# Performance work log

Hardware: AMD Instinct MI355X
Metric: run time of the kernel (lower is better)

## Reference

```python
import jax, jax.numpy as jnp
import numpy as np

V = 50257   # vocab
P = 2048    # max positions
D = 768     # hidden
H = 12      # heads
F = 3072    # 4*D ffn
NL = 12     # layers
L = 2048    # seq len
EPS = 1e-5


def setup_inputs() -> dict:
    key = jax.random.key(0)
    ks = jax.random.split(key, 12)
    r = lambda k, shp: jax.random.normal(k, shp, jnp.float32) * 0.02
    return dict(
        input_ids=jax.random.randint(ks[0], (1, L), 0, V, dtype=jnp.int32),
        attention_mask=jnp.ones((1, L), jnp.int32),
        wte=r(ks[1], (V, D)),
        wpe=r(ks[2], (P, D)),
        lnf_w=jnp.ones((D,), jnp.float32),
        lnf_b=jnp.zeros((D,), jnp.float32),
        ln1_w=jnp.ones((NL, D), jnp.float32),
        ln1_b=jnp.zeros((NL, D), jnp.float32),
        qw=r(ks[3], (NL, D, D)),
        kw=r(ks[4], (NL, D, D)),
        vw=r(ks[5], (NL, D, D)),
        ow=r(ks[6], (NL, D, D)),
        ob=jnp.zeros((NL, D), jnp.float32),
        ln2_w=jnp.ones((NL, D), jnp.float32),
        ln2_b=jnp.zeros((NL, D), jnp.float32),
        fcw=r(ks[7], (NL, D, F)),
        fcb=jnp.zeros((NL, F), jnp.float32),
        pw=r(ks[8], (NL, F, D)),
        pb=jnp.zeros((NL, D), jnp.float32),
    )


def _ln(x, w, b):
    mu = jnp.mean(x, -1, keepdims=True)
    var = jnp.mean((x - mu) ** 2, -1, keepdims=True)
    return (x - mu) * jax.lax.rsqrt(var + EPS) * w + b


def reference(input_ids, attention_mask, wte, wpe, lnf_w, lnf_b,
              ln1_w, ln1_b, qw, kw, vw, ow, ob, ln2_w, ln2_b,
              fcw, fcb, pw, pb):
    ids = input_ids.reshape(-1, input_ids.shape[-1])          # [1, L]
    pos = jnp.cumsum(attention_mask, -1) - 1
    pos = jnp.where(attention_mask == 0, 1, pos)
    h = (wte[ids] + wpe[pos])[0]                               # [L, D]

    key_valid = attention_mask[0] > 0                          # actual_length mask
    mask = jnp.tril(jnp.ones((L, L), bool)) & key_valid[None, :]  # causal+pad
    dh = D // H

    def layer(h, p):
        l1w, l1b, Wq, Wk, Wv, Wo, bo, l2w, l2b, Wf, bf, Wp, bp = p
        x = _ln(h, l1w, l1b)
        q = (x @ Wq).reshape(L, H, dh)
        k = (x @ Wk).reshape(L, H, dh)
        v = (x @ Wv).reshape(L, H, dh)
        # GPT-Neo attention: NO 1/sqrt(dh) scaling
        scores = jnp.einsum('qhd,khd->hqk', q, k)
        scores = jnp.where(mask[None], scores, jnp.float32(-1e9))
        attn = jax.nn.softmax(scores, axis=-1)
        ctx = jnp.einsum('hqk,khd->qhd', attn, v).reshape(L, D)
        h = h + ctx @ Wo + bo
        y = _ln(h, l2w, l2b)
        h = h + jax.nn.gelu(y @ Wf + bf, approximate=True) @ Wp + bp
        return h, None

    h, _ = jax.lax.scan(layer, h, (ln1_w, ln1_b, qw, kw, vw, ow, ob,
                                   ln2_w, ln2_b, fcw, fcb, pw, pb))
    return _ln(h[None, :, :], lnf_w, lnf_b)                    # [1, L, D]
```

## Files before the change

kernel.cpp:

```cpp
#include <hip/hip_runtime.h>
#include <hip/hip_bf16.h>
#include <math.h>
#include <stdint.h>

#define L 2048
#define D 768
#define H 12
#define DH 64
#define F 3072
#define NL 12
#define QKVN 2304

typedef __attribute__((ext_vector_type(8))) short bf16x8;
typedef __attribute__((ext_vector_type(4))) float f32x4;

__device__ __forceinline__ ushort f2bf(float x) {
    union { float f; uint32_t u; } c; c.f = x;
    uint32_t r = c.u + 0x7FFFu + ((c.u >> 16) & 1u);
    return (ushort)(r >> 16);
}

__device__ __forceinline__ uint32_t cvt_pk_bf16(float lo, float hi) {
    uint32_t r;
    asm("v_cvt_pk_bf16_f32 %0, %1, %2" : "=v"(r) : "v"(lo), "v"(hi));
    return r;
}

__device__ __forceinline__ bf16x8 ldfrag(const ushort* p) {
    ushort4 lo = *(const ushort4*)(p);
    ushort4 hi = *(const ushort4*)(p + 16);
    bf16x8 f;
    f[0] = (short)lo.x; f[1] = (short)lo.y; f[2] = (short)lo.z; f[3] = (short)lo.w;
    f[4] = (short)hi.x; f[5] = (short)hi.y; f[6] = (short)hi.z; f[7] = (short)hi.w;
    return f;
}

__device__ __forceinline__ float gelu_tanh(float x) {
    float c = 0.7978845608028654f;
    float inner = c * (x + 0.044715f * x * x * x);
    return 0.5f * x * (1.0f + tanhf(inner));
}

__global__ void pos_kernel(const int* __restrict__ mask, int* __restrict__ pos) {
    __shared__ int sm[L];
    for (int i = threadIdx.x; i < L; i += blockDim.x) sm[i] = mask[i];
    __syncthreads();
    int t = blockIdx.x * blockDim.x + threadIdx.x;
    if (t < L) {
        int s = 0;
        for (int j = 0; j <= t; ++j) s += sm[j];
        int p = s - 1;
        if (sm[t] == 0) p = 1;
        pos[t] = p;
    }
}

__global__ void maskb_kernel(const int* __restrict__ mask, float* __restrict__ mb) {
    int i = blockIdx.x * blockDim.x + threadIdx.x;
    if (i < L) mb[i] = mask[i] ? 0.f : -1e9f;
}

__global__ __launch_bounds__(256) void embed_kernel(const int* __restrict__ ids,
                                                    const int* __restrict__ pos,
                                                    const float* __restrict__ wte,
                                                    const float* __restrict__ wpe,
                                                    float* __restrict__ h) {
    int t = blockIdx.x;
    int id = ids[t];
    int p = pos[t];
    const float* we = wte + (size_t)id * D;
    const float* wp = wpe + (size_t)p * D;
    float* hr = h + (size_t)t * D;
#pragma unroll
    for (int i = 0; i < 3; ++i) {
        int d = threadIdx.x + i * 256;
        hr[d] = we[d] + wp[d];
    }
}

template <bool OUTBF>
__global__ __launch_bounds__(256) void ln_kernel(const float* __restrict__ in,
                                                 const float* __restrict__ w,
                                                 const float* __restrict__ b,
                                                 float* __restrict__ outF,
                                                 ushort* __restrict__ outB) {
    __shared__ float red[2][4];
    int row = blockIdx.x;
    const float* x = in + (size_t)row * D;
    int t = threadIdx.x;
    float v0 = x[t], v1 = x[t + 256], v2 = x[t + 512];
    float s = v0 + v1 + v2;
    float ss = v0 * v0 + v1 * v1 + v2 * v2;
#pragma unroll
    for (int o = 32; o; o >>= 1) {
        s += __shfl_xor(s, o);
        ss += __shfl_xor(ss, o);
    }
    int wave = t >> 6;
    if ((t & 63) == 0) { red[0][wave] = s; red[1][wave] = ss; }
    __syncthreads();
    s = red[0][0] + red[0][1] + red[0][2] + red[0][3];
    ss = red[1][0] + red[1][1] + red[1][2] + red[1][3];
    float mean = s * (1.f / D);
    float var = ss * (1.f / D) - mean * mean;
    float rstd = rsqrtf(var + 1e-5f);
#pragma unroll
    for (int i = 0; i < 3; ++i) {
        int d = t + i * 256;
        float vv = (i == 0) ? v0 : (i == 1) ? v1 : v2;
        float y = (vv - mean) * rstd * w[d] + b[d];
        if (OUTBF) outB[(size_t)row * D + d] = f2bf(y);
        else       outF[(size_t)row * D + d] = y;
    }
}

template <int S, bool OUTBF>
__global__ __launch_bounds__(256) void redln_kernel(const float* __restrict__ part,
                                                    const float* __restrict__ bias,
                                                    float* __restrict__ h,
                                                    const float* __restrict__ lnw,
                                                    const float* __restrict__ lnb,
                                                    ushort* __restrict__ outB,
                                                    float* __restrict__ outF) {
    __shared__ float red[2][4];
    int row = blockIdx.x;
    int t = threadIdx.x;
    float v[3];
    float s = 0.f, ss = 0.f;
#pragma unroll
    for (int i = 0; i < 3; ++i) {
        int d = t + i * 256;
        float x = h[(size_t)row * D + d] + bias[d];
#pragma unroll
        for (int sp = 0; sp < S; ++sp)
            x += part[((size_t)sp * L + row) * D + d];
        v[i] = x;
        h[(size_t)row * D + d] = x;
        s += x;
        ss += x * x;
    }
#pragma unroll
    for (int o = 32; o; o >>= 1) {
        s += __shfl_xor(s, o);
        ss += __shfl_xor(ss, o);
    }
    int wave = t >> 6;
    if ((t & 63) == 0) { red[0][wave] = s; red[1][wave] = ss; }
    __syncthreads();
    s = red[0][0] + red[0][1] + red[0][2] + red[0][3];
    ss = red[1][0] + red[1][1] + red[1][2] + red[1][3];
    float mean = s * (1.f / D);
    float var = ss * (1.f / D) - mean * mean;
    float rstd = rsqrtf(var + 1e-5f);
#pragma unroll
    for (int i = 0; i < 3; ++i) {
        int d = t + i * 256;
        float y = (v[i] - mean) * rstd * lnw[d] + lnb[d];
        if (OUTBF) outB[(size_t)row * D + d] = f2bf(y);
        else       outF[(size_t)row * D + d] = y;
    }
}

__global__ __launch_bounds__(256) void tcast_f32(const float* __restrict__ in,
                                                 ushort* __restrict__ out,
                                                 int K, int N,
                                                 size_t inStride, size_t outStride) {
    in += blockIdx.z * inStride;
    out += blockIdx.z * outStride;
    __shared__ float tile[64][65];
    int k0 = blockIdx.y * 64, n0 = blockIdx.x * 64;
    int t = threadIdx.x;
    int cl = t & 63, rg = t >> 6;
#pragma unroll
    for (int i = 0; i < 16; ++i) {
        int r = rg + 4 * i;
        tile[r][cl] = in[(size_t)(k0 + r) * N + n0 + cl];
    }
    __syncthreads();
#pragma unroll
    for (int i = 0; i < 16; ++i) {
        int r = rg + 4 * i;
        out[(size_t)(n0 + r) * K + k0 + cl] = f2bf(tile[cl][r]);
    }
}

template <int ACT, bool OUTBF, int SPLITK, bool VSPLIT>
__global__ __launch_bounds__(256) void gemm_bf16(const ushort* __restrict__ A,
                                                 const ushort* __restrict__ Bt,
                                                 const float* __restrict__ bias,
                                                 const float* __restrict__ resid,
                                                 float* __restrict__ outF,
                                                 ushort* __restrict__ outB,
                                                 float* __restrict__ pout,
                                                 ushort* __restrict__ vTout,
                                                 int M, int N, int K) {
    __shared__ __align__(16) char lds[32768];
    const int tid = threadIdx.x;
    const int lane = tid & 63, w = tid >> 6;
    const int wr = w >> 1, wc = w & 1;
    const int bm = blockIdx.y * 128, bn = blockIdx.x * 128;
    const int l15 = lane & 15, l4 = lane >> 4;
    const int srow = tid >> 2, c = tid & 3;
    const int blo = (c & 1) * 32 + (c >> 1) * 8;
    const int kLen = K / SPLITK;
    const int kStart = (SPLITK > 1) ? blockIdx.z * kLen : 0;

    const int sxor = (srow & 3) << 4;
    const int wo0 = srow * 64 + (blo ^ sxor);
    const int wo1 = srow * 64 + ((blo + 16) ^ sxor);
    const int rxor = (l4 * 16) ^ ((l15 & 3) << 4);
    const int aBase = (wr * 64 + l15) * 64 + rxor;
    const int bBase = (wc * 64 + l15) * 64 + rxor;

    f32x4 acc[4][4];
#pragma unroll
    for (int m = 0; m < 4; ++m)
#pragma unroll
        for (int n = 0; n < 4; ++n)
            acc[m][n] = (f32x4){0.f, 0.f, 0.f, 0.f};

    const ushort* Ag = A + (size_t)(bm + srow) * K + kStart + c * 8;
    const ushort* Ag2 = Ag + (size_t)64 * K;
    const ushort* Bg = Bt + (size_t)(bn + srow) * K + kStart + c * 8;
    const ushort* Bg2 = Bg + (size_t)64 * K;

    uint4 a0 = *(const uint4*)(Ag);
    uint4 a1 = *(const uint4*)(Ag2);
    uint4 b0 = *(const uint4*)(Bg);
    uint4 b1 = *(const uint4*)(Bg2);

    for (int k0 = 0; k0 < kLen; k0 += 32) {
        char* Ab = lds + ((k0 >> 5) & 1) * 16384;
        char* Bb = Ab + 8192;
        uint2 t0, t1;
        t0.x = a0.x; t0.y = a0.y; t1.x = a0.z; t1.y = a0.w;
        *(uint2*)(Ab + wo0) = t0;
        *(uint2*)(Ab + wo1) = t1;
        t0.x = a1.x; t0.y = a1.y; t1.x = a1.z; t1.y = a1.w;
        *(uint2*)(Ab + wo0 + 4096) = t0;
        *(uint2*)(Ab + wo1 + 4096) = t1;
        t0.x = b0.x; t0.y = b0.y; t1.x = b0.z; t1.y = b0.w;
        *(uint2*)(Bb + wo0) = t0;
        *(uint2*)(Bb + wo1) = t1;
        t0.x = b1.x; t0.y = b1.y; t1.x = b1.z; t1.y = b1.w;
        *(uint2*)(Bb + wo0 + 4096) = t0;
        *(uint2*)(Bb + wo1 + 4096) = t1;
        __syncthreads();
        if (k0 + 32 < kLen) {
            a0 = *(const uint4*)(Ag + k0 + 32);
            a1 = *(const uint4*)(Ag2 + k0 + 32);
            b0 = *(const uint4*)(Bg + k0 + 32);
            b1 = *(const uint4*)(Bg2 + k0 + 32);
        }
        bf16x8 af[4], bfv[4];
#pragma unroll
        for (int m = 0; m < 4; ++m)
            af[m] = *(const bf16x8*)(Ab + aBase + m * 1024);
#pragma unroll
        for (int n = 0; n < 4; ++n)
            bfv[n] = *(const bf16x8*)(Bb + bBase + n * 1024);
#pragma unroll
        for (int m = 0; m < 4; ++m)
#pragma unroll
            for (int n = 0; n < 4; ++n)
                acc[m][n] = __builtin_amdgcn_mfma_f32_16x16x32_bf16(af[m], bfv[n], acc[m][n], 0, 0, 0);
    }

    if (SPLITK > 1) {
        const size_t sb = (size_t)blockIdx.z * M;
#pragma unroll
        for (int m = 0; m < 4; ++m)
#pragma unroll
            for (int n = 0; n < 4; ++n) {
                int col = bn + wc * 64 + n * 16 + l15;
#pragma unroll
                for (int r = 0; r < 4; ++r) {
                    int row = bm + wr * 64 + m * 16 + l4 * 4 + r;
                    pout[(sb + row) * N + col] = acc[m][n][r];
                }
            }
    } else {
#pragma unroll
        for (int m = 0; m < 4; ++m)
#pragma unroll
            for (int n = 0; n < 4; ++n) {
                int col = bn + wc * 64 + n * 16 + l15;
                int row0 = bm + wr * 64 + m * 16 + l4 * 4;
                if (VSPLIT && col >= 2 * D) {
                    ushort4 pk;
                    pk.x = f2bf(acc[m][n][0]);
                    pk.y = f2bf(acc[m][n][1]);
                    pk.z = f2bf(acc[m][n][2]);
                    pk.w = f2bf(acc[m][n][3]);
                    *(ushort4*)(vTout + (size_t)(col - 2 * D) * L + row0) = pk;
                } else {
#pragma unroll
                    for (int r = 0; r < 4; ++r) {
                        int row = row0 + r;
                        float v = acc[m][n][r];
                        if (bias) v += bias[col];
                        if (ACT == 1) v = gelu_tanh(v);
                        if (resid) v += resid[(size_t)row * N + col];
                        if (OUTBF) outB[(size_t)row * N + col] = f2bf(v);
                        else       outF[(size_t)row * N + col] = v;
                    }
                }
            }
    }
}

__global__ __launch_bounds__(256) void attn_kernel(const ushort* __restrict__ qkv,
                                                   const ushort* __restrict__ vT,
                                                   const float* __restrict__ maskb,
                                                   ushort* __restrict__ ctx) {
    __shared__ __align__(16) char Kl[2][8192];
    __shared__ __align__(16) char Vl[2][8192];
    __shared__ float Ml[2][64];
    const int hh = blockIdx.y;
    const int q0 = ((int)gridDim.x - 1 - (int)blockIdx.x) * 64;
    const int tid = threadIdx.x;
    const int lane = tid & 63, w = tid >> 6;
    const int l15 = lane & 15, l4 = lane >> 4;
    const int qg = q0 + w * 16 + l15;
    const int qmin = q0 + w * 16;

    bf16x8 qf[2];
#pragma unroll
    for (int ks = 0; ks < 2; ++ks)
        qf[ks] = ldfrag(qkv + (size_t)qg * QKVN + hh * 64 + ks * 32 + l4 * 4);

    f32x4 o[4];
#pragma unroll
    for (int i = 0; i < 4; ++i) o[i] = (f32x4){0.f, 0.f, 0.f, 0.f};
    float mrun = -1e30f, lrun = 0.f;

    const int srow = tid >> 2, c = tid & 3;
    const int blo = (c & 1) * 32 + (c >> 1) * 8;
    const int swz = (srow & 7) << 4;
    const int rb = srow * 128;
    const int lo4 = blo & 15;
    const int s0 = rb + (((blo)      & 0x70) ^ swz) + lo4;
    const int s1 = rb + (((blo + 16) & 0x70) ^ swz) + lo4;
    const int s2 = rb + (((blo + 64) & 0x70) ^ swz) + lo4;
    const int s3 = rb + (((blo + 80) & 0x70) ^ swz) + lo4;
    const int fxor = (l15 & 7) << 4;

    const ushort* Ksrc = qkv + (size_t)srow * QKVN + D + hh * 64 + c * 8;
    const ushort* Vsrc = vT + (size_t)(hh * 64 + srow) * L + c * 8;

    uint4 ka, kb, va, vb;
    float mv = 0.f;
    const int nt = q0 / 64 + 1;

    {
        ka = *(const uint4*)(Ksrc);
        kb = *(const uint4*)(Ksrc + 32);
        va = *(const uint4*)(Vsrc);
        vb = *(const uint4*)(Vsrc + 32);
        if (tid < 64) mv = maskb[tid];
    }

    for (int it = 0; it < nt; ++it) {
        const int kv0 = it * 64;
        const int b = it & 1;
        {
            char* Kb = Kl[b];
            char* Vb = Vl[b];
            uint2 t0, t1;
            t0.x = ka.x; t0.y = ka.y; t1.x = ka.z; t1.y = ka.w;
            *(uint2*)(Kb + s0) = t0;
            *(uint2*)(Kb + s1) = t1;
            t0.x = kb.x; t0.y = kb.y; t1.x = kb.z; t1.y = kb.w;
            *(uint2*)(Kb + s2) = t0;
            *(uint2*)(Kb + s3) = t1;
            t0.x = va.x; t0.y = va.y; t1.x = va.z; t1.y = va.w;
            *(uint2*)(Vb + s0) = t0;
            *(uint2*)(Vb + s1) = t1;
            t0.x = vb.x; t0.y = vb.y; t1.x = vb.z; t1.y = vb.w;
            *(uint2*)(Vb + s2) = t0;
            *(uint2*)(Vb + s3) = t1;
            if (tid < 64) Ml[b][tid] = mv;
        }
        __syncthreads();
        if (it + 1 < nt) {
            const size_t koff = (size_t)(kv0 + 64) * QKVN;
            ka = *(const uint4*)(Ksrc + koff);
            kb = *(const uint4*)(Ksrc + koff + 32);
            va = *(const uint4*)(Vsrc + kv0 + 64);
            vb = *(const uint4*)(Vsrc + kv0 + 96);
            if (tid < 64) mv = maskb[kv0 + 64 + tid];
        }

        const char* Kb = Kl[b];
        const char* Vb = Vl[b];

        f32x4 st[4];
#pragma unroll
        for (int m = 0; m < 4; ++m) st[m] = (f32x4){0.f, 0.f, 0.f, 0.f};
#pragma unroll
        for (int m = 0; m < 4; ++m)
#pragma unroll
            for (int ks = 0; ks < 2; ++ks) {
                bf16x8 kf = *(const bf16x8*)(Kb + (m * 16 + l15) * 128 +
                                             ((ks * 64 + l4 * 16) ^ fxor));
                st[m] = __builtin_amdgcn_mfma_f32_16x16x32_bf16(kf, qf[ks], st[m], 0, 0, 0);
            }

        float p[4][4];
        float tmax = -1e30f;
        const bool full = (kv0 + 63 <= qmin);
        if (full) {
#pragma unroll
            for (int m = 0; m < 4; ++m)
#pragma unroll
                for (int r = 0; r < 4; ++r) {
                    int kl = m * 16 + l4 * 4 + r;
                    float s = st[m][r] + Ml[b][kl];
                    p[m][r] = s;
                    tmax = fmaxf(tmax, s);
                }
        } else {
#pragma unroll
            for (int m = 0; m < 4; ++m)
#pragma unroll
                for (int r = 0; r < 4; ++r) {
                    int kl = m * 16 + l4 * 4 + r;
                    float s = st[m][r] + Ml[b][kl];
                    if (kv0 + kl > qg) s = -1e30f;
                    p[m][r] = s;
                    tmax = fmaxf(tmax, s);
                }
        }
        tmax = fmaxf(tmax, __shfl_xor(tmax, 16));
        tmax = fmaxf(tmax, __shfl_xor(tmax, 32));
        const bool noresc = __all(tmax <= mrun);
        float mnew = noresc ? mrun : fmaxf(mrun, tmax);
        float scale = noresc ? 1.f : __expf(mrun - mnew);
        float ts = 0.f;
#pragma unroll
        for (int m = 0; m < 4; ++m)
#pragma unroll
            for (int r = 0; r < 4; ++r) {
                float e = __expf(p[m][r] - mnew);
                p[m][r] = e;
                ts += e;
            }
        ts += __shfl_xor(ts, 16);
        ts += __shfl_xor(ts, 32);
        lrun = lrun * scale + ts;
        mrun = mnew;

        bf16x8 pf[2];
#pragma unroll
        for (int g = 0; g < 2; ++g) {
            union { bf16x8 v; uint32_t d[4]; } pu;
            pu.d[0] = cvt_pk_bf16(p[2 * g][0], p[2 * g][1]);
            pu.d[1] = cvt_pk_bf16(p[2 * g][2], p[2 * g][3]);
            pu.d[2] = cvt_pk_bf16(p[2 * g + 1][0], p[2 * g + 1][1]);
            pu.d[3] = cvt_pk_bf16(p[2 * g + 1][2], p[2 * g + 1][3]);
            pf[g] = pu.v;
        }
        if (!noresc) {
#pragma unroll
            for (int i = 0; i < 4; ++i) {
                o[i][0] *= scale; o[i][1] *= scale; o[i][2] *= scale; o[i][3] *= scale;
            }
        }
#pragma unroll
        for (int dhb = 0; dhb < 4; ++dhb)
#pragma unroll
            for (int g = 0; g < 2; ++g) {
                bf16x8 vf = *(const bf16x8*)(Vb + (dhb * 16 + l15) * 128 +
                                             ((g * 64 + l4 * 16) ^ fxor));
                o[dhb] = __builtin_amdgcn_mfma_f32_16x16x32_bf16(vf, pf[g], o[dhb], 0, 0, 0);
            }
    }

    float rinv = 1.0f / lrun;
#pragma unroll
    for (int dhb = 0; dhb < 4; ++dhb) {
        ushort4 pk;
        pk.x = f2bf(o[dhb][0] * rinv);
        pk.y = f2bf(o[dhb][1] * rinv);
        pk.z = f2bf(o[dhb][2] * rinv);
        pk.w = f2bf(o[dhb][3] * rinv);
        *(ushort4*)(ctx + (size_t)qg * D + hh * 64 + dhb * 16 + l4 * 4) = pk;
    }
}

extern "C" void kernel_launch(void* const* d_in, const int* in_sizes, int n_in,
                              void* d_out, int out_size, void* d_ws, size_t ws_size,
                              hipStream_t stream) {
    const int* ids = (const int*)d_in[0];
    const int* amask = (const int*)d_in[1];
    const float* wte = (const float*)d_in[2];
    const float* wpe = (const float*)d_in[3];
    const float* lnf_w = (const float*)d_in[4];
    const float* lnf_b = (const float*)d_in[5];
    const float* ln1_w = (const float*)d_in[6];
    const float* ln1_b = (const float*)d_in[7];
    const float* qw = (const float*)d_in[8];
    const float* kw = (const float*)d_in[9];
    const float* vw = (const float*)d_in[10];
    const float* ow = (const float*)d_in[11];
    const float* ob = (const float*)d_in[12];
    const float* ln2_w = (const float*)d_in[13];
    const float* ln2_b = (const float*)d_in[14];
    const float* fcw = (const float*)d_in[15];
    const float* fcb = (const float*)d_in[16];
    const float* pw = (const float*)d_in[17];
    const float* pb = (const float*)d_in[18];

    char* p = (char*)d_ws;
    auto take = [&](size_t bytes) -> char* {
        char* r = p;
        p += (bytes + 4095) & ~(size_t)4095;
        return r;
    };
    ushort* wqkvT = (ushort*)take((size_t)NL * QKVN * D * 2);
    ushort* woT   = (ushort*)take((size_t)NL * D * D * 2);
    ushort* fcwT  = (ushort*)take((size_t)NL * F * D * 2);
    ushort* pwT   = (ushort*)take((size_t)NL * D * F * 2);
    float*  h     = (float*)take((size_t)L * D * 4);
    ushort* xb    = (ushort*)take((size_t)L * D * 2);
    ushort* qkvb  = (ushort*)take((size_t)L * QKVN * 2);
    ushort* vTb   = (ushort*)take((size_t)D * L * 2);
    ushort* ctxb  = (ushort*)take((size_t)L * D * 2);
    ushort* f1b   = (ushort*)take((size_t)L * F * 2);
    float*  pk    = (float*)take((size_t)4 * L * D * 4);
    float*  mb    = (float*)take(L * 4);
    int*    pos   = (int*)take(L * 4);

    pos_kernel<<<8, 256, 0, stream>>>(amask, pos);
    maskb_kernel<<<8, 256, 0, stream>>>(amask, mb);
    embed_kernel<<<L, 256, 0, stream>>>(ids, pos, wte, wpe, h);

    tcast_f32<<<dim3(12, 12, NL), 256, 0, stream>>>(qw, wqkvT, D, D,
                                                    (size_t)D * D, (size_t)QKVN * D);
    tcast_f32<<<dim3(12, 12, NL), 256, 0, stream>>>(kw, wqkvT + (size_t)D * D, D, D,
                                                    (size_t)D * D, (size_t)QKVN * D);
    tcast_f32<<<dim3(12, 12, NL), 256, 0, stream>>>(vw, wqkvT + (size_t)2 * D * D, D, D,
                                                    (size_t)D * D, (size_t)QKVN * D);
    tcast_f32<<<dim3(12, 12, NL), 256, 0, stream>>>(ow, woT, D, D,
                                                    (size_t)D * D, (size_t)D * D);
    tcast_f32<<<dim3(48, 12, NL), 256, 0, stream>>>(fcw, fcwT, D, F,
                                                    (size_t)D * F, (size_t)F * D);
    tcast_f32<<<dim3(12, 48, NL), 256, 0, stream>>>(pw, pwT, F, D,
                                                    (size_t)F * D, (size_t)D * F);

    ln_kernel<true><<<L, 256, 0, stream>>>(h, ln1_w, ln1_b, nullptr, xb);

    for (int l = 0; l < NL; ++l) {
        gemm_bf16<0, true, 1, true><<<dim3(QKVN / 128, L / 128), 256, 0, stream>>>(
            xb, wqkvT + (size_t)l * QKVN * D, nullptr, nullptr, nullptr, qkvb, nullptr,
            vTb, L, QKVN, D);
        attn_kernel<<<dim3(L / 64, H), 256, 0, stream>>>(qkvb, vTb, mb, ctxb);
        gemm_bf16<0, true, 4, false><<<dim3(D / 128, L / 128, 4), 256, 0, stream>>>(
            ctxb, woT + (size_t)l * D * D, nullptr, nullptr, nullptr, nullptr, pk,
            nullptr, L, D, D);
        redln_kernel<4, true><<<L, 256, 0, stream>>>(
            pk, ob + l * D, h, ln2_w + l * D, ln2_b + l * D, xb, nullptr);
        gemm_bf16<1, true, 1, false><<<dim3(F / 128, L / 128), 256, 0, stream>>>(
            xb, fcwT + (size_t)l * F * D, fcb + l * F, nullptr, nullptr, f1b, nullptr,
            nullptr, L, F, D);
        gemm_bf16<0, true, 4, false><<<dim3(D / 128, L / 128, 4), 256, 0, stream>>>(
            f1b, pwT + (size_t)l * D * F, nullptr, nullptr, nullptr, nullptr, pk,
            nullptr, L, D, F);
        if (l < NL - 1) {
            redln_kernel<4, true><<<L, 256, 0, stream>>>(
                pk, pb + l * D, h, ln1_w + (l + 1) * D, ln1_b + (l + 1) * D, xb, nullptr);
        } else {
            redln_kernel<4, false><<<L, 256, 0, stream>>>(
                pk, pb + l * D, h, lnf_w, lnf_b, nullptr, (float*)d_out);
        }
    }
}
```

Measured before the change: 1.919 ms.

## Replace split-K projections with 64x64 GEMM fusing bias+residual; halve attention query tile

The attention output projection and the FFN down projection no longer use 4-way split-K GEMMs that write fp32 partial sums for a separate reduce-plus-LayerNorm kernel. A new 64x64-tile GEMM with K-step 64 adds the bias and the residual directly into h, and a plain LayerNorm kernel follows. This removes the write and read-back of four L×D fp32 partial buffers per projection. In exchange each block does longer K loops with smaller tiles and less data reuse. The attention kernel now handles 32 queries per block with 128 threads, doubling the block count for better CU fill and causal load balance.

```diff
diff --git a/kernel.cpp b/kernel.cpp
--- a/kernel.cpp
+++ b/kernel.cpp
@@ -114,53 +114,6 @@
     }
 }
 
-template <int S, bool OUTBF>
-__global__ __launch_bounds__(256) void redln_kernel(const float* __restrict__ part,
-                                                    const float* __restrict__ bias,
-                                                    float* __restrict__ h,
-                                                    const float* __restrict__ lnw,
-                                                    const float* __restrict__ lnb,
-                                                    ushort* __restrict__ outB,
-                                                    float* __restrict__ outF) {
-    __shared__ float red[2][4];
-    int row = blockIdx.x;
-    int t = threadIdx.x;
-    float v[3];
-    float s = 0.f, ss = 0.f;
-#pragma unroll
-    for (int i = 0; i < 3; ++i) {
-        int d = t + i * 256;
-        float x = h[(size_t)row * D + d] + bias[d];
-#pragma unroll
-        for (int sp = 0; sp < S; ++sp)
-            x += part[((size_t)sp * L + row) * D + d];
-        v[i] = x;
-        h[(size_t)row * D + d] = x;
-        s += x;
-        ss += x * x;
-    }
-#pragma unroll
-    for (int o = 32; o; o >>= 1) {
-        s += __shfl_xor(s, o);
-        ss += __shfl_xor(ss, o);
-    }
-    int wave = t >> 6;
-    if ((t & 63) == 0) { red[0][wave] = s; red[1][wave] = ss; }
-    __syncthreads();
-    s = red[0][0] + red[0][1] + red[0][2] + red[0][3];
-    ss = red[1][0] + red[1][1] + red[1][2] + red[1][3];
-    float mean = s * (1.f / D);
-    float var = ss * (1.f / D) - mean * mean;
-    float rstd = rsqrtf(var + 1e-5f);
-#pragma unroll
-    for (int i = 0; i < 3; ++i) {
-        int d = t + i * 256;
-        float y = (v[i] - mean) * rstd * lnw[d] + lnb[d];
-        if (OUTBF) outB[(size_t)row * D + d] = f2bf(y);
-        else       outF[(size_t)row * D + d] = y;
-    }
-}
-
 __global__ __launch_bounds__(256) void tcast_f32(const float* __restrict__ in,
                                                  ushort* __restrict__ out,
                                                  int K, int N,
@@ -184,14 +137,13 @@
     }
 }
 
-template <int ACT, bool OUTBF, int SPLITK, bool VSPLIT>
+template <int ACT, bool OUTBF, bool VSPLIT>
 __global__ __launch_bounds__(256) void gemm_bf16(const ushort* __restrict__ A,
                                                  const ushort* __restrict__ Bt,
                                                  const float* __restrict__ bias,
                                                  const float* __restrict__ resid,
                                                  float* __restrict__ outF,
                                                  ushort* __restrict__ outB,
-                                                 float* __restrict__ pout,
                                                  ushort* __restrict__ vTout,
                                                  int M, int N, int K) {
     __shared__ __align__(16) char lds[32768];
@@ -202,8 +154,6 @@
     const int l15 = lane & 15, l4 = lane >> 4;
     const int srow = tid >> 2, c = tid & 3;
     const int blo = (c & 1) * 32 + (c >> 1) * 8;
-    const int kLen = K / SPLITK;
-    const int kStart = (SPLITK > 1) ? blockIdx.z * kLen : 0;
 
     const int sxor = (srow & 3) << 4;
     const int wo0 = srow * 64 + (blo ^ sxor);
@@ -219,9 +169,9 @@
         for (int n = 0; n < 4; ++n)
             acc[m][n] = (f32x4){0.f, 0.f, 0.f, 0.f};
 
-    const ushort* Ag = A + (size_t)(bm + srow) * K + kStart + c * 8;
+    const ushort* Ag = A + (size_t)(bm + srow) * K + c * 8;
     const ushort* Ag2 = Ag + (size_t)64 * K;
-    const ushort* Bg = Bt + (size_t)(bn + srow) * K + kStart + c * 8;
+    const ushort* Bg = Bt + (size_t)(bn + srow) * K + c * 8;
     const ushort* Bg2 = Bg + (size_t)64 * K;
 
     uint4 a0 = *(const uint4*)(Ag);
@@ -229,7 +179,7 @@
     uint4 b0 = *(const uint4*)(Bg);
     uint4 b1 = *(const uint4*)(Bg2);
 
-    for (int k0 = 0; k0 < kLen; k0 += 32) {
+    for (int k0 = 0; k0 < K; k0 += 32) {
         char* Ab = lds + ((k0 >> 5) & 1) * 16384;
         char* Bb = Ab + 8192;
         uint2 t0, t1;
@@ -246,7 +196,7 @@
         *(uint2*)(Bb + wo0 + 4096) = t0;
         *(uint2*)(Bb + wo1 + 4096) = t1;
         __syncthreads();
-        if (k0 + 32 < kLen) {
+        if (k0 + 32 < K) {
             a0 = *(const uint4*)(Ag + k0 + 32);
             a1 = *(const uint4*)(Ag2 + k0 + 32);
             b0 = *(const uint4*)(Bg + k0 + 32);
@@ -266,50 +216,136 @@
                 acc[m][n] = __builtin_amdgcn_mfma_f32_16x16x32_bf16(af[m], bfv[n], acc[m][n], 0, 0, 0);
     }
 
-    if (SPLITK > 1) {
-        const size_t sb = (size_t)blockIdx.z * M;
-#pragma unroll
-        for (int m = 0; m < 4; ++m)
-#pragma unroll
-            for (int n = 0; n < 4; ++n) {
-                int col = bn + wc * 64 + n * 16 + l15;
+#pragma unroll
+    for (int m = 0; m < 4; ++m)
+#pragma unroll
+        for (int n = 0; n < 4; ++n) {
+            int col = bn + wc * 64 + n * 16 + l15;
+            int row0 = bm + wr * 64 + m * 16 + l4 * 4;
+            if (VSPLIT && col >= 2 * D) {
+                ushort4 pk;
+                pk.x = f2bf(acc[m][n][0]);
+                pk.y = f2bf(acc[m][n][1]);
+                pk.z = f2bf(acc[m][n][2]);
+                pk.w = f2bf(acc[m][n][3]);
+                *(ushort4*)(vTout + (size_t)(col - 2 * D) * L + row0) = pk;
+            } else {
 #pragma unroll
                 for (int r = 0; r < 4; ++r) {
-                    int row = bm + wr * 64 + m * 16 + l4 * 4 + r;
-                    pout[(sb + row) * N + col] = acc[m][n][r];
+                    int row = row0 + r;
+                    float v = acc[m][n][r];
+                    if (bias) v += bias[col];
+                    if (ACT == 1) v = gelu_tanh(v);
+                    if (resid) v += resid[(size_t)row * N + col];
+                    if (OUTBF) outB[(size_t)row * N + col] = f2bf(v);
+                    else       outF[(size_t)row * N + col] = v;
                 }
             }
-    } else {
-#pragma unroll
-        for (int m = 0; m < 4; ++m)
-#pragma unroll
-            for (int n = 0; n < 4; ++n) {
-                int col = bn + wc * 64 + n * 16 + l15;
-                int row0 = bm + wr * 64 + m * 16 + l4 * 4;
-                if (VSPLIT && col >= 2 * D) {
-                    ushort4 pk;
-                    pk.x = f2bf(acc[m][n][0]);
-                    pk.y = f2bf(acc[m][n][1]);
-                    pk.z = f2bf(acc[m][n][2]);
-                    pk.w = f2bf(acc[m][n][3]);
-                    *(ushort4*)(vTout + (size_t)(col - 2 * D) * L + row0) = pk;
-                } else {
-#pragma unroll
-                    for (int r = 0; r < 4; ++r) {
-                        int row = row0 + r;
-                        float v = acc[m][n][r];
-                        if (bias) v += bias[col];
-                        if (ACT == 1) v = gelu_tanh(v);
-                        if (resid) v += resid[(size_t)row * N + col];
-                        if (OUTBF) outB[(size_t)row * N + col] = f2bf(v);
-                        else       outF[(size_t)row * N + col] = v;
-                    }
-                }
-            }
-    }
-}
-
-__global__ __launch_bounds__(256) void attn_kernel(const ushort* __restrict__ qkv,
+        }
+}
+
+__global__ __launch_bounds__(256) void gemm64_bf16(const ushort* __restrict__ A,
+                                                   const ushort* __restrict__ Bt,
+                                                   const float* __restrict__ bias,
+                                                   float* __restrict__ h,
+                                                   int M, int N, int K) {
+    __shared__ __align__(16) char lds[32768];
+    const int tid = threadIdx.x;
+    const int lane = tid & 63, w = tid >> 6;
+    const int wr = w >> 1, wc = w & 1;
+    const int bm = blockIdx.y * 64, bn = blockIdx.x * 64;
+    const int l15 = lane & 15, l4 = lane >> 4;
+    const int srow = tid >> 2, q = tid & 3;
+    const int swz = (srow & 7) << 4;
+    const int rb = srow * 128;
+    int offlo[2], offhi[2];
+#pragma unroll
+    for (int i = 0; i < 2; ++i) {
+        int g = 2 * q + i;
+        int cc = g & 3, hf = g >> 2;
+        int blo = (cc & 1) * 32 + ((cc >> 1) & 1) * 8 + hf * 64;
+        offlo[i] = rb + ((blo & 0x70) ^ swz) + (blo & 15);
+        int bhi = blo + 16;
+        offhi[i] = rb + ((bhi & 0x70) ^ swz) + (bhi & 15);
+    }
+    const int fxor = (l15 & 7) << 4;
+
+    f32x4 acc[2][2];
+#pragma unroll
+    for (int m = 0; m < 2; ++m)
+#pragma unroll
+        for (int n = 0; n < 2; ++n)
+            acc[m][n] = (f32x4){0.f, 0.f, 0.f, 0.f};
+
+    const ushort* Ag = A + (size_t)(bm + srow) * K + q * 16;
+    const ushort* Bg = Bt + (size_t)(bn + srow) * K + q * 16;
+
+    uint4 a0 = *(const uint4*)(Ag);
+    uint4 a1 = *(const uint4*)(Ag + 8);
+    uint4 b0 = *(const uint4*)(Bg);
+    uint4 b1 = *(const uint4*)(Bg + 8);
+
+    for (int k0 = 0; k0 < K; k0 += 64) {
+        char* Ab = lds + ((k0 >> 6) & 1) * 16384;
+        char* Bb = Ab + 8192;
+        uint2 t0, t1;
+        t0.x = a0.x; t0.y = a0.y; t1.x = a0.z; t1.y = a0.w;
+        *(uint2*)(Ab + offlo[0]) = t0;
+        *(uint2*)(Ab + offhi[0]) = t1;
+        t0.x = a1.x; t0.y = a1.y; t1.x = a1.z; t1.y = a1.w;
+        *(uint2*)(Ab + offlo[1]) = t0;
+        *(uint2*)(Ab + offhi[1]) = t1;
+        t0.x = b0.x; t0.y = b0.y; t1.x = b0.z; t1.y = b0.w;
+        *(uint2*)(Bb + offlo[0]) = t0;
+        *(uint2*)(Bb + offhi[0]) = t1;
+        t0.x = b1.x; t0.y = b1.y; t1.x = b1.z; t1.y = b1.w;
+        *(uint2*)(Bb + offlo[1]) = t0;
+        *(uint2*)(Bb + offhi[1]) = t1;
+        __syncthreads();
+        if (k0 + 64 < K) {
+            a0 = *(const uint4*)(Ag + k0 + 64);
+            a1 = *(const uint4*)(Ag + k0 + 72);
+            b0 = *(const uint4*)(Bg + k0 + 64);
+            b1 = *(const uint4*)(Bg + k0 + 72);
+        }
+        bf16x8 af[2][2], bfv[2][2];
+#pragma unroll
+        for (int m = 0; m < 2; ++m)
+#pragma unroll
+            for (int ks = 0; ks < 2; ++ks)
+                af[m][ks] = *(const bf16x8*)(Ab + (wr * 32 + m * 16 + l15) * 128 +
+                                             ((ks * 64 + l4 * 16) ^ fxor));
+#pragma unroll
+        for (int n = 0; n < 2; ++n)
+#pragma unroll
+            for (int ks = 0; ks < 2; ++ks)
+                bfv[n][ks] = *(const bf16x8*)(Bb + (wc * 32 + n * 16 + l15) * 128 +
+                                              ((ks * 64 + l4 * 16) ^ fxor));
+#pragma unroll
+        for (int m = 0; m < 2; ++m)
+#pragma unroll
+            for (int n = 0; n < 2; ++n)
+#pragma unroll
+                for (int ks = 0; ks < 2; ++ks)
+                    acc[m][n] = __builtin_amdgcn_mfma_f32_16x16x32_bf16(
+                        af[m][ks], bfv[n][ks], acc[m][n], 0, 0, 0);
+    }
+
+#pragma unroll
+    for (int m = 0; m < 2; ++m)
+#pragma unroll
+        for (int n = 0; n < 2; ++n) {
+            int col = bn + wc * 32 + n * 16 + l15;
+#pragma unroll
+            for (int r = 0; r < 4; ++r) {
+                int row = bm + wr * 32 + m * 16 + l4 * 4 + r;
+                float v = acc[m][n][r] + bias[col] + h[(size_t)row * N + col];
+                h[(size_t)row * N + col] = v;
+            }
+        }
+}
+
+__global__ __launch_bounds__(128) void attn_kernel(const ushort* __restrict__ qkv,
                                                    const ushort* __restrict__ vT,
                                                    const float* __restrict__ maskb,
                                                    ushort* __restrict__ ctx) {
@@ -317,7 +353,7 @@
     __shared__ __align__(16) char Vl[2][8192];
     __shared__ float Ml[2][64];
     const int hh = blockIdx.y;
-    const int q0 = ((int)gridDim.x - 1 - (int)blockIdx.x) * 64;
+    const int q0 = ((int)gridDim.x - 1 - (int)blockIdx.x) * 32;
     const int tid = threadIdx.x;
     const int lane = tid & 63, w = tid >> 6;
     const int l15 = lane & 15, l4 = lane >> 4;
@@ -334,31 +370,32 @@
     for (int i = 0; i < 4; ++i) o[i] = (f32x4){0.f, 0.f, 0.f, 0.f};
     float mrun = -1e30f, lrun = 0.f;
 
-    const int srow = tid >> 2, c = tid & 3;
-    const int blo = (c & 1) * 32 + (c >> 1) * 8;
+    const int srow = tid >> 1, hf = tid & 1;
     const int swz = (srow & 7) << 4;
     const int rb = srow * 128;
-    const int lo4 = blo & 15;
-    const int s0 = rb + (((blo)      & 0x70) ^ swz) + lo4;
-    const int s1 = rb + (((blo + 16) & 0x70) ^ swz) + lo4;
-    const int s2 = rb + (((blo + 64) & 0x70) ^ swz) + lo4;
-    const int s3 = rb + (((blo + 80) & 0x70) ^ swz) + lo4;
+    int offlo[4], offhi[4];
+#pragma unroll
+    for (int cc = 0; cc < 4; ++cc) {
+        int blo = (cc & 1) * 32 + ((cc >> 1) & 1) * 8 + hf * 64;
+        offlo[cc] = rb + ((blo & 0x70) ^ swz) + (blo & 15);
+        int bhi = blo + 16;
+        offhi[cc] = rb + ((bhi & 0x70) ^ swz) + (bhi & 15);
+    }
     const int fxor = (l15 & 7) << 4;
 
-    const ushort* Ksrc = qkv + (size_t)srow * QKVN + D + hh * 64 + c * 8;
-    const ushort* Vsrc = vT + (size_t)(hh * 64 + srow) * L + c * 8;
-
-    uint4 ka, kb, va, vb;
+    const ushort* Ksrc = qkv + (size_t)srow * QKVN + D + hh * 64 + hf * 32;
+    const ushort* Vsrc = vT + (size_t)(hh * 64 + srow) * L + hf * 32;
+
+    uint4 kx[4], vx[4];
     float mv = 0.f;
     const int nt = q0 / 64 + 1;
 
-    {
-        ka = *(const uint4*)(Ksrc);
-        kb = *(const uint4*)(Ksrc + 32);
-        va = *(const uint4*)(Vsrc);
-        vb = *(const uint4*)(Vsrc + 32);
-        if (tid < 64) mv = maskb[tid];
-    }
+#pragma unroll
+    for (int cc = 0; cc < 4; ++cc) {
+        kx[cc] = *(const uint4*)(Ksrc + cc * 8);
+        vx[cc] = *(const uint4*)(Vsrc + cc * 8);
+    }
+    if (tid < 64) mv = maskb[tid];
 
     for (int it = 0; it < nt; ++it) {
         const int kv0 = it * 64;
@@ -367,27 +404,25 @@
             char* Kb = Kl[b];
             char* Vb = Vl[b];
             uint2 t0, t1;
-            t0.x = ka.x; t0.y = ka.y; t1.x = ka.z; t1.y = ka.w;
-            *(uint2*)(Kb + s0) = t0;
-            *(uint2*)(Kb + s1) = t1;
-            t0.x = kb.x; t0.y = kb.y; t1.x = kb.z; t1.y = kb.w;
-            *(uint2*)(Kb + s2) = t0;
-            *(uint2*)(Kb + s3) = t1;
-            t0.x = va.x; t0.y = va.y; t1.x = va.z; t1.y = va.w;
-            *(uint2*)(Vb + s0) = t0;
-            *(uint2*)(Vb + s1) = t1;
-            t0.x = vb.x; t0.y = vb.y; t1.x = vb.z; t1.y = vb.w;
-            *(uint2*)(Vb + s2) = t0;
-            *(uint2*)(Vb + s3) = t1;
+#pragma unroll
+            for (int cc = 0; cc < 4; ++cc) {
+                t0.x = kx[cc].x; t0.y = kx[cc].y; t1.x = kx[cc].z; t1.y = kx[cc].w;
+                *(uint2*)(Kb + offlo[cc]) = t0;
+                *(uint2*)(Kb + offhi[cc]) = t1;
+                t0.x = vx[cc].x; t0.y = vx[cc].y; t1.x = vx[cc].z; t1.y = vx[cc].w;
+                *(uint2*)(Vb + offlo[cc]) = t0;
+                *(uint2*)(Vb + offhi[cc]) = t1;
+            }
             if (tid < 64) Ml[b][tid] = mv;
         }
         __syncthreads();
         if (it + 1 < nt) {
             const size_t koff = (size_t)(kv0 + 64) * QKVN;
-            ka = *(const uint4*)(Ksrc + koff);
-            kb = *(const uint4*)(Ksrc + koff + 32);
-            va = *(const uint4*)(Vsrc + kv0 + 64);
-            vb = *(const uint4*)(Vsrc + kv0 + 96);
+#pragma unroll
+            for (int cc = 0; cc < 4; ++cc) {
+                kx[cc] = *(const uint4*)(Ksrc + koff + cc * 8);
+                vx[cc] = *(const uint4*)(Vsrc + kv0 + 64 + cc * 8);
+            }
             if (tid < 64) mv = maskb[kv0 + 64 + tid];
         }
 
@@ -527,7 +562,6 @@
     ushort* vTb   = (ushort*)take((size_t)D * L * 2);
     ushort* ctxb  = (ushort*)take((size_t)L * D * 2);
     ushort* f1b   = (ushort*)take((size_t)L * F * 2);
-    float*  pk    = (float*)take((size_t)4 * L * D * 4);
     float*  mb    = (float*)take(L * 4);
     int*    pos   = (int*)take(L * 4);
 
@@ -551,27 +585,25 @@
     ln_kernel<true><<<L, 256, 0, stream>>>(h, ln1_w, ln1_b, nullptr, xb);
 
     for (int l = 0; l < NL; ++l) {
-        gemm_bf16<0, true, 1, true><<<dim3(QKVN / 128, L / 128), 256, 0, stream>>>(
-            xb, wqkvT + (size_t)l * QKVN * D, nullptr, nullptr, nullptr, qkvb, nullptr,
+        gemm_bf16<0, true, true><<<dim3(QKVN / 128, L / 128), 256, 0, stream>>>(
+            xb, wqkvT + (size_t)l * QKVN * D, nullptr, nullptr, nullptr, qkvb,
             vTb, L, QKVN, D);
-        attn_kernel<<<dim3(L / 64, H), 256, 0, stream>>>(qkvb, vTb, mb, ctxb);
-        gemm_bf16<0, true, 4, false><<<dim3(D / 128, L / 128, 4), 256, 0, stream>>>(
-            ctxb, woT + (size_t)l * D * D, nullptr, nullptr, nullptr, nullptr, pk,
-            nullptr, L, D, D);
-        redln_kernel<4, true><<<L, 256, 0, stream>>>(
-            pk, ob + l * D, h, ln2_w + l * D, ln2_b + l * D, xb, nullptr);
-        gemm_bf16<1, true, 1, false><<<dim3(F / 128, L / 128), 256, 0, stream>>>(
-            xb, fcwT + (size_t)l * F * D, fcb + l * F, nullptr, nullptr, f1b, nullptr,
+        attn_kernel<<<dim3(L / 32, H), 128, 0, stream>>>(qkvb, vTb, mb, ctxb);
+        gemm64_bf16<<<dim3(D / 64, L / 64), 256, 0, stream>>>(
+            ctxb, woT + (size_t)l * D * D, ob + l * D, h, L, D, D);
+        ln_kernel<true><<<L, 256, 0, stream>>>(h, ln2_w + l * D, ln2_b + l * D,
+                                               nullptr, xb);
+        gemm_bf16<1, true, false><<<dim3(F / 128, L / 128), 256, 0, stream>>>(
+            xb, fcwT + (size_t)l * F * D, fcb + l * F, nullptr, nullptr, f1b,
             nullptr, L, F, D);
-        gemm_bf16<0, true, 4, false><<<dim3(D / 128, L / 128, 4), 256, 0, stream>>>(
-            f1b, pwT + (size_t)l * D * F, nullptr, nullptr, nullptr, nullptr, pk,
-            nullptr, L, D, F);
+        gemm64_bf16<<<dim3(D / 64, L / 64), 256, 0, stream>>>(
+            f1b, pwT + (size_t)l * D * F, pb + l * D, h, L, D, F);
         if (l < NL - 1) {
-            redln_kernel<4, true><<<L, 256, 0, stream>>>(
-                pk, pb + l * D, h, ln1_w + (l + 1) * D, ln1_b + (l + 1) * D, xb, nullptr);
+            ln_kernel<true><<<L, 256, 0, stream>>>(h, ln1_w + (l + 1) * D,
+                                                   ln1_b + (l + 1) * D, nullptr, xb);
         } else {
-            redln_kernel<4, false><<<L, 256, 0, stream>>>(
-                pk, pb + l * D, h, lnf_w, lnf_b, nullptr, (float*)d_out);
-        }
-    }
-}
+            ln_kernel<false><<<L, 256, 0, stream>>>(h, lnf_w, lnf_b,
+                                                    (float*)d_out, nullptr);
+        }
+    }
+}
```

Result: slower. 2.084 ms (+8.6%).

## Split causal attention along the KV axis into two partitions with a combine kernel

Applied to the files above, without the earlier changes.

The attention kernel now takes a split index from blockIdx.z and processes only its half of the causal KV tiles. It writes unnormalised fp32 partial outputs plus the running max and sum per query. A new combine kernel merges the two partials with log-sum-exp rescaling and writes the bf16 context. The aim is to cut the critical path of the longest causal query blocks and to raise the block count above the CU count. In exchange it adds an extra kernel launch and fp32 partial-buffer traffic on every layer.

```diff
diff --git a/kernel.cpp b/kernel.cpp
--- a/kernel.cpp
+++ b/kernel.cpp
@@ -309,14 +309,18 @@
     }
 }
 
+template <int NS>
 __global__ __launch_bounds__(256) void attn_kernel(const ushort* __restrict__ qkv,
                                                    const ushort* __restrict__ vT,
                                                    const float* __restrict__ maskb,
-                                                   ushort* __restrict__ ctx) {
+                                                   float* __restrict__ po,
+                                                   float* __restrict__ pm,
+                                                   float* __restrict__ pl) {
     __shared__ __align__(16) char Kl[2][8192];
     __shared__ __align__(16) char Vl[2][8192];
     __shared__ float Ml[2][64];
     const int hh = blockIdx.y;
+    const int sp = blockIdx.z;
     const int q0 = ((int)gridDim.x - 1 - (int)blockIdx.x) * 64;
     const int tid = threadIdx.x;
     const int lane = tid & 63, w = tid >> 6;
@@ -324,167 +328,215 @@
     const int qg = q0 + w * 16 + l15;
     const int qmin = q0 + w * 16;
 
-    bf16x8 qf[2];
-#pragma unroll
-    for (int ks = 0; ks < 2; ++ks)
-        qf[ks] = ldfrag(qkv + (size_t)qg * QKVN + hh * 64 + ks * 32 + l4 * 4);
+    const int nt = q0 / 64 + 1;
+    const int chunk = (nt + NS - 1) / NS;
+    const int it0 = sp * chunk;
+    int it1 = it0 + chunk;
+    if (it1 > nt) it1 = nt;
 
     f32x4 o[4];
 #pragma unroll
     for (int i = 0; i < 4; ++i) o[i] = (f32x4){0.f, 0.f, 0.f, 0.f};
     float mrun = -1e30f, lrun = 0.f;
 
-    const int srow = tid >> 2, c = tid & 3;
-    const int blo = (c & 1) * 32 + (c >> 1) * 8;
-    const int swz = (srow & 7) << 4;
-    const int rb = srow * 128;
-    const int lo4 = blo & 15;
-    const int s0 = rb + (((blo)      & 0x70) ^ swz) + lo4;
-    const int s1 = rb + (((blo + 16) & 0x70) ^ swz) + lo4;
-    const int s2 = rb + (((blo + 64) & 0x70) ^ swz) + lo4;
-    const int s3 = rb + (((blo + 80) & 0x70) ^ swz) + lo4;
-    const int fxor = (l15 & 7) << 4;
-
-    const ushort* Ksrc = qkv + (size_t)srow * QKVN + D + hh * 64 + c * 8;
-    const ushort* Vsrc = vT + (size_t)(hh * 64 + srow) * L + c * 8;
-
-    uint4 ka, kb, va, vb;
-    float mv = 0.f;
-    const int nt = q0 / 64 + 1;
-
-    {
-        ka = *(const uint4*)(Ksrc);
-        kb = *(const uint4*)(Ksrc + 32);
-        va = *(const uint4*)(Vsrc);
-        vb = *(const uint4*)(Vsrc + 32);
-        if (tid < 64) mv = maskb[tid];
-    }
-
-    for (int it = 0; it < nt; ++it) {
-        const int kv0 = it * 64;
-        const int b = it & 1;
+    if (it0 < it1) {
+        bf16x8 qf[2];
+#pragma unroll
+        for (int ks = 0; ks < 2; ++ks)
+            qf[ks] = ldfrag(qkv + (size_t)qg * QKVN + hh * 64 + ks * 32 + l4 * 4);
+
+        const int srow = tid >> 2, c = tid & 3;
+        const int blo = (c & 1) * 32 + (c >> 1) * 8;
+        const int swz = (srow & 7) << 4;
+        const int rb = srow * 128;
+        const int lo4 = blo & 15;
+        const int s0 = rb + (((blo)      & 0x70) ^ swz) + lo4;
+        const int s1 = rb + (((blo + 16) & 0x70) ^ swz) + lo4;
+        const int s2 = rb + (((blo + 64) & 0x70) ^ swz) + lo4;
+        const int s3 = rb + (((blo + 80) & 0x70) ^ swz) + lo4;
+        const int fxor = (l15 & 7) << 4;
+
+        const ushort* Ksrc = qkv + (size_t)srow * QKVN + D + hh * 64 + c * 8;
+        const ushort* Vsrc = vT + (size_t)(hh * 64 + srow) * L + c * 8;
+
+        uint4 ka, kb, va, vb;
+        float mv = 0.f;
         {
-            char* Kb = Kl[b];
-            char* Vb = Vl[b];
-            uint2 t0, t1;
-            t0.x = ka.x; t0.y = ka.y; t1.x = ka.z; t1.y = ka.w;
-            *(uint2*)(Kb + s0) = t0;
-            *(uint2*)(Kb + s1) = t1;
-            t0.x = kb.x; t0.y = kb.y; t1.x = kb.z; t1.y = kb.w;
-            *(uint2*)(Kb + s2) = t0;
-            *(uint2*)(Kb + s3) = t1;
-            t0.x = va.x; t0.y = va.y; t1.x = va.z; t1.y = va.w;
-            *(uint2*)(Vb + s0) = t0;
-            *(uint2*)(Vb + s1) = t1;
-            t0.x = vb.x; t0.y = vb.y; t1.x = vb.z; t1.y = vb.w;
-            *(uint2*)(Vb + s2) = t0;
-            *(uint2*)(Vb + s3) = t1;
-            if (tid < 64) Ml[b][tid] = mv;
-        }
-        __syncthreads();
-        if (it + 1 < nt) {
-            const size_t koff = (size_t)(kv0 + 64) * QKVN;
+            const size_t koff = (size_t)(it0 * 64) * QKVN;
             ka = *(const uint4*)(Ksrc + koff);
             kb = *(const uint4*)(Ksrc + koff + 32);
-            va = *(const uint4*)(Vsrc + kv0 + 64);
-            vb = *(const uint4*)(Vsrc + kv0 + 96);
-            if (tid < 64) mv = maskb[kv0 + 64 + tid];
+            va = *(const uint4*)(Vsrc + it0 * 64);
+            vb = *(const uint4*)(Vsrc + it0 * 64 + 32);
+            if (tid < 64) mv = maskb[it0 * 64 + tid];
         }
 
-        const char* Kb = Kl[b];
-        const char* Vb = Vl[b];
-
-        f32x4 st[4];
-#pragma unroll
-        for (int m = 0; m < 4; ++m) st[m] = (f32x4){0.f, 0.f, 0.f, 0.f};
-#pragma unroll
-        for (int m = 0; m < 4; ++m)
-#pragma unroll
-            for (int ks = 0; ks < 2; ++ks) {
-                bf16x8 kf = *(const bf16x8*)(Kb + (m * 16 + l15) * 128 +
-                                             ((ks * 64 + l4 * 16) ^ fxor));
-                st[m] = __builtin_amdgcn_mfma_f32_16x16x32_bf16(kf, qf[ks], st[m], 0, 0, 0);
+        for (int it = it0; it < it1; ++it) {
+            const int kv0 = it * 64;
+            const int b = it & 1;
+            {
+                char* Kb = Kl[b];
+                char* Vb = Vl[b];
+                uint2 t0, t1;
+                t0.x = ka.x; t0.y = ka.y; t1.x = ka.z; t1.y = ka.w;
+                *(uint2*)(Kb + s0) = t0;
+                *(uint2*)(Kb + s1) = t1;
+                t0.x = kb.x; t0.y = kb.y; t1.x = kb.z; t1.y = kb.w;
+                *(uint2*)(Kb + s2) = t0;
+                *(uint2*)(Kb + s3) = t1;
+                t0.x = va.x; t0.y = va.y; t1.x = va.z; t1.y = va.w;
+                *(uint2*)(Vb + s0) = t0;
+                *(uint2*)(Vb + s1) = t1;
+                t0.x = vb.x; t0.y = vb.y; t1.x = vb.z; t1.y = vb.w;
+                *(uint2*)(Vb + s2) = t0;
+                *(uint2*)(Vb + s3) = t1;
+                if (tid < 64) Ml[b][tid] = mv;
             }
-
-        float p[4][4];
-        float tmax = -1e30f;
-        const bool full = (kv0 + 63 <= qmin);
-        if (full) {
+            __syncthreads();
+            if (it + 1 < it1) {
+                const size_t koff = (size_t)(kv0 + 64) * QKVN;
+                ka = *(const uint4*)(Ksrc + koff);
+                kb = *(const uint4*)(Ksrc + koff + 32);
+                va = *(const uint4*)(Vsrc + kv0 + 64);
+                vb = *(const uint4*)(Vsrc + kv0 + 96);
+                if (tid < 64) mv = maskb[kv0 + 64 + tid];
+            }
+
+            const char* Kb = Kl[b];
+            const char* Vb = Vl[b];
+
+            f32x4 st[4];
+#pragma unroll
+            for (int m = 0; m < 4; ++m) st[m] = (f32x4){0.f, 0.f, 0.f, 0.f};
 #pragma unroll
             for (int m = 0; m < 4; ++m)
 #pragma unroll
+                for (int ks = 0; ks < 2; ++ks) {
+                    bf16x8 kf = *(const bf16x8*)(Kb + (m * 16 + l15) * 128 +
+                                                 ((ks * 64 + l4 * 16) ^ fxor));
+                    st[m] = __builtin_amdgcn_mfma_f32_16x16x32_bf16(kf, qf[ks], st[m], 0, 0, 0);
+                }
+
+            float p[4][4];
+            float tmax = -1e30f;
+            const bool full = (kv0 + 63 <= qmin);
+            if (full) {
+#pragma unroll
+                for (int m = 0; m < 4; ++m)
+#pragma unroll
+                    for (int r = 0; r < 4; ++r) {
+                        int kl = m * 16 + l4 * 4 + r;
+                        float s = st[m][r] + Ml[b][kl];
+                        p[m][r] = s;
+                        tmax = fmaxf(tmax, s);
+                    }
+            } else {
+#pragma unroll
+                for (int m = 0; m < 4; ++m)
+#pragma unroll
+                    for (int r = 0; r < 4; ++r) {
+                        int kl = m * 16 + l4 * 4 + r;
+                        float s = st[m][r] + Ml[b][kl];
+                        if (kv0 + kl > qg) s = -1e30f;
+                        p[m][r] = s;
+                        tmax = fmaxf(tmax, s);
+                    }
+            }
+            tmax = fmaxf(tmax, __shfl_xor(tmax, 16));
+            tmax = fmaxf(tmax, __shfl_xor(tmax, 32));
+            const bool noresc = __all(tmax <= mrun);
+            float mnew = noresc ? mrun : fmaxf(mrun, tmax);
+            float scale = noresc ? 1.f : __expf(mrun - mnew);
+            float ts = 0.f;
+#pragma unroll
+            for (int m = 0; m < 4; ++m)
+#pragma unroll
                 for (int r = 0; r < 4; ++r) {
-                    int kl = m * 16 + l4 * 4 + r;
-                    float s = st[m][r] + Ml[b][kl];
-                    p[m][r] = s;
-                    tmax = fmaxf(tmax, s);
+                    float e = __expf(p[m][r] - mnew);
+                    p[m][r] = e;
+                    ts += e;
                 }
-        } else {
-#pragma unroll
-            for (int m = 0; m < 4; ++m)
-#pragma unroll
-                for (int r = 0; r < 4; ++r) {
-                    int kl = m * 16 + l4 * 4 + r;
-                    float s = st[m][r] + Ml[b][kl];
-                    if (kv0 + kl > qg) s = -1e30f;
-                    p[m][r] = s;
-                    tmax = fmaxf(tmax, s);
+            ts += __shfl_xor(ts, 16);
+            ts += __shfl_xor(ts, 32);
+            lrun = lrun * scale + ts;
+            mrun = mnew;
+
+            bf16x8 pf[2];
+#pragma unroll
+            for (int g = 0; g < 2; ++g) {
+                union { bf16x8 v; uint32_t d[4]; } pu;
+                pu.d[0] = cvt_pk_bf16(p[2 * g][0], p[2 * g][1]);
+                pu.d[1] = cvt_pk_bf16(p[2 * g][2], p[2 * g][3]);
+                pu.d[2] = cvt_pk_bf16(p[2 * g + 1][0], p[2 * g + 1][1]);
+                pu.d[3] = cvt_pk_bf16(p[2 * g + 1][2], p[2 * g + 1][3]);
+                pf[g] = pu.v;
+            }
+            if (!noresc) {
+#pragma unroll
+                for (int i = 0; i < 4; ++i) {
+                    o[i][0] *= scale; o[i][1] *= scale; o[i][2] *= scale; o[i][3] *= scale;
+                }
+            }
+#pragma unroll
+            for (int dhb = 0; dhb < 4; ++dhb)
+#pragma unroll
+                for (int g = 0; g < 2; ++g) {
+                    bf16x8 vf = *(const bf16x8*)(Vb + (dhb * 16 + l15) * 128 +
+                                                 ((g * 64 + l4 * 16) ^ fxor));
+                    o[dhb] = __builtin_amdgcn_mfma_f32_16x16x32_bf16(vf, pf[g], o[dhb], 0, 0, 0);
                 }
         }
-        tmax = fmaxf(tmax, __shfl_xor(tmax, 16));
-        tmax = fmaxf(tmax, __shfl_xor(tmax, 32));
-        const bool noresc = __all(tmax <= mrun);
-        float mnew = noresc ? mrun : fmaxf(mrun, tmax);
-        float scale = noresc ? 1.f : __expf(mrun - mnew);
-        float ts = 0.f;
-#pragma unroll
-        for (int m = 0; m < 4; ++m)
-#pragma unroll
-            for (int r = 0; r < 4; ++r) {
-                float e = __expf(p[m][r] - mnew);
-                p[m][r] = e;
-                ts += e;
-            }
-        ts += __shfl_xor(ts, 16);
-        ts += __shfl_xor(ts, 32);
-        lrun = lrun * scale + ts;
-        mrun = mnew;
-
-        bf16x8 pf[2];
-#pragma unroll
-        for (int g = 0; g < 2; ++g) {
-            union { bf16x8 v; uint32_t d[4]; } pu;
-            pu.d[0] = cvt_pk_bf16(p[2 * g][0], p[2 * g][1]);
-            pu.d[1] = cvt_pk_bf16(p[2 * g][2], p[2 * g][3]);
-            pu.d[2] = cvt_pk_bf16(p[2 * g + 1][0], p[2 * g + 1][1]);
-            pu.d[3] = cvt_pk_bf16(p[2 * g + 1][2], p[2 * g + 1][3]);
-            pf[g] = pu.v;
+    }
+
+    const size_t pb = (size_t)(sp * H + hh) * L + qg;
+    if (l4 == 0) { pm[pb] = mrun; pl[pb] = lrun; }
+    float* op = po + pb * 64;
+#pragma unroll
+    for (int dhb = 0; dhb < 4; ++dhb)
+        *(f32x4*)(op + dhb * 16 + l4 * 4) = o[dhb];
+}
+
+template <int NS>
+__global__ __launch_bounds__(256) void attn_combine(const float* __restrict__ po,
+                                                    const float* __restrict__ pm,
+                                                    const float* __restrict__ pl,
+                                                    ushort* __restrict__ ctx) {
+    const int hh = blockIdx.y;
+    const int q = blockIdx.x * 64 + (threadIdx.x >> 2);
+    const int d0 = (threadIdx.x & 3) * 16;
+    size_t idx[NS];
+    float mm = -1e30f;
+#pragma unroll
+    for (int s = 0; s < NS; ++s) {
+        idx[s] = (size_t)(s * H + hh) * L + q;
+        mm = fmaxf(mm, pm[idx[s]]);
+    }
+    float e[NS];
+    float l = 0.f;
+#pragma unroll
+    for (int s = 0; s < NS; ++s) {
+        e[s] = __expf(pm[idx[s]] - mm);
+        l += pl[idx[s]] * e[s];
+    }
+    float rinv = 1.0f / l;
+    ushort* cp = ctx + (size_t)q * D + hh * 64 + d0;
+#pragma unroll
+    for (int j = 0; j < 16; j += 4) {
+        float acc[4] = {0.f, 0.f, 0.f, 0.f};
+#pragma unroll
+        for (int s = 0; s < NS; ++s) {
+            const float* op = po + idx[s] * 64 + d0 + j;
+            float4 v = *(const float4*)op;
+            acc[0] += v.x * e[s];
+            acc[1] += v.y * e[s];
+            acc[2] += v.z * e[s];
+            acc[3] += v.w * e[s];
         }
-        if (!noresc) {
-#pragma unroll
-            for (int i = 0; i < 4; ++i) {
-                o[i][0] *= scale; o[i][1] *= scale; o[i][2] *= scale; o[i][3] *= scale;
-            }
-        }
-#pragma unroll
-        for (int dhb = 0; dhb < 4; ++dhb)
-#pragma unroll
-            for (int g = 0; g < 2; ++g) {
-                bf16x8 vf = *(const bf16x8*)(Vb + (dhb * 16 + l15) * 128 +
-                                             ((g * 64 + l4 * 16) ^ fxor));
-                o[dhb] = __builtin_amdgcn_mfma_f32_16x16x32_bf16(vf, pf[g], o[dhb], 0, 0, 0);
-            }
-    }
-
-    float rinv = 1.0f / lrun;
-#pragma unroll
-    for (int dhb = 0; dhb < 4; ++dhb) {
         ushort4 pk;
-        pk.x = f2bf(o[dhb][0] * rinv);
-        pk.y = f2bf(o[dhb][1] * rinv);
-        pk.z = f2bf(o[dhb][2] * rinv);
-        pk.w = f2bf(o[dhb][3] * rinv);
-        *(ushort4*)(ctx + (size_t)qg * D + hh * 64 + dhb * 16 + l4 * 4) = pk;
+        pk.x = f2bf(acc[0] * rinv);
+        pk.y = f2bf(acc[1] * rinv);
+        pk.z = f2bf(acc[2] * rinv);
+        pk.w = f2bf(acc[3] * rinv);
+        *(ushort4*)(cp + j) = pk;
     }
 }
 
@@ -528,6 +580,9 @@
     ushort* ctxb  = (ushort*)take((size_t)L * D * 2);
     ushort* f1b   = (ushort*)take((size_t)L * F * 2);
     float*  pk    = (float*)take((size_t)4 * L * D * 4);
+    float*  po    = (float*)take((size_t)2 * H * L * 64 * 4);
+    float*  pm    = (float*)take((size_t)2 * H * L * 4);
+    float*  pl    = (float*)take((size_t)2 * H * L * 4);
     float*  mb    = (float*)take(L * 4);
     int*    pos   = (int*)take(L * 4);
 
@@ -554,7 +609,9 @@
         gemm_bf16<0, true, 1, true><<<dim3(QKVN / 128, L / 128), 256, 0, stream>>>(
             xb, wqkvT + (size_t)l * QKVN * D, nullptr, nullptr, nullptr, qkvb, nullptr,
             vTb, L, QKVN, D);
-        attn_kernel<<<dim3(L / 64, H), 256, 0, stream>>>(qkvb, vTb, mb, ctxb);
+        attn_kernel<2><<<dim3(L / 64, H, 2), 256, 0, stream>>>(qkvb, vTb, mb,
+                                                               po, pm, pl);
+        attn_combine<2><<<dim3(L / 64, H), 256, 0, stream>>>(po, pm, pl, ctxb);
         gemm_bf16<0, true, 4, false><<<dim3(D / 128, L / 128, 4), 256, 0, stream>>>(
             ctxb, woT + (size_t)l * D * D, nullptr, nullptr, nullptr, nullptr, pk,
             nullptr, L, D, D);
```

Measured after the change: 1.825 ms. -4.9%, faster.
